# Kernel tuning notes

Hardware: AMD Instinct MI355X
Metric: run time of the kernel (lower is better)

The kernel has to match this reference:

```python
import jax, jax.numpy as jnp
import numpy as np

B, N, M = 8, 2048, 2048
DQ = DK = DV = H = O = 1024

def setup_inputs() -> dict:
    key = jax.random.key(0)
    ks = jax.random.split(key, 10)
    input_query = jax.random.normal(ks[0], (B, N, DQ), dtype=jnp.float32)
    input_key = jax.random.normal(ks[1], (B, M, DK), dtype=jnp.float32)
    input_value = jax.random.normal(ks[2], (B, M, DV), dtype=jnp.float32)
    seq_lens = jax.random.randint(ks[3], (B,), 1, M + 1)
    seq_lens = seq_lens.at[0].set(M)  # original asserts max(seq_lens) == M
    s = 1.0 / np.sqrt(DQ)
    Wq = jax.random.normal(ks[4], (DQ, H), dtype=jnp.float32) * s
    bq = jnp.zeros((H,), dtype=jnp.float32)
    Wk = jax.random.normal(ks[5], (DK, H), dtype=jnp.float32) * s
    bk = jnp.zeros((H,), dtype=jnp.float32)
    Wv = jax.random.normal(ks[6], (DV, O), dtype=jnp.float32) * s
    bv = jnp.zeros((O,), dtype=jnp.float32)
    return {"input_query": input_query, "input_key": input_key, "input_value": input_value,
            "seq_lens": seq_lens, "Wq": Wq, "bq": bq, "Wk": Wk, "bk": bk, "Wv": Wv, "bv": bv}


def reference(input_query, input_key, input_value, seq_lens, Wq, bq, Wk, bk, Wv, bv):
    hidden_dim = Wq.shape[1]
    lq = input_query @ Wq + bq          # (B, N, H)
    lk = input_key @ Wk + bk            # (B, M, H)
    lv = input_value @ Wv + bv          # (B, M, O)
    scores = jnp.einsum('bnh,bmh->bnm', lq, lk) / jnp.sqrt(jnp.float32(hidden_dim))
    # additive mask: 0 for valid positions, finfo.min for padded (as in original)
    valid = (jnp.arange(scores.shape[-1]) < seq_lens[:, None])[:, None, :]  # (B,1,M)
    add_mask = jnp.where(valid, 0.0, jnp.finfo(scores.dtype).min)
    scores = scores + add_mask
    probs = jax.nn.softmax(scores, axis=-1)
    out = jnp.einsum('bnm,bmo->bno', probs, lv)  # dropout is identity in eval
    return out
```

## Files before the change

kernel.cpp:

```cpp
#include <hip/hip_runtime.h>
#include <hip/hip_bf16.h>

typedef unsigned short u16;
typedef __attribute__((ext_vector_type(8))) short bfrag;
typedef __attribute__((ext_vector_type(4))) float f32x4;
typedef __attribute__((ext_vector_type(8))) unsigned short us8;
typedef __attribute__((ext_vector_type(4))) unsigned short us4;

__device__ __forceinline__ u16 f2bf(float f) {
  union { float f; unsigned int u; } x; x.f = f;
  unsigned int r = x.u + 0x7fffu + ((x.u >> 16) & 1u);
  return (u16)(r >> 16);
}
__device__ __forceinline__ float bf2f(u16 u) {
  union { unsigned int u; float f; } x; x.u = ((unsigned int)u) << 16;
  return x.f;
}

__device__ __forceinline__ void gld16(const void* g, void* l) {
  __builtin_amdgcn_global_load_lds((const __attribute__((address_space(1))) void*)g,
                                   (__attribute__((address_space(3))) void*)l, 16, 0, 0);
}

__global__ __launch_bounds__(256) void transpose_w(const float* __restrict__ W0,
                                                   const float* __restrict__ W1,
                                                   const float* __restrict__ W2,
                                                   u16* __restrict__ T0,
                                                   u16* __restrict__ T1,
                                                   u16* __restrict__ T2) {
  const float* W = (blockIdx.z == 0) ? W0 : ((blockIdx.z == 1) ? W1 : W2);
  u16* T = (blockIdx.z == 0) ? T0 : ((blockIdx.z == 1) ? T1 : T2);
  __shared__ u16 tile[64][72];
  const int t = threadIdx.x;
  const int rr = t >> 4;
  const int cc = (t & 15) * 4;
  const int kbase = blockIdx.y * 64, nbase = blockIdx.x * 64;
#pragma unroll
  for (int j = 0; j < 4; ++j) {
    int kl = rr + j * 16;
    float4 v = *(const float4*)(W + (size_t)(kbase + kl) * 1024 + nbase + cc);
    tile[kl][cc + 0] = f2bf(v.x);
    tile[kl][cc + 1] = f2bf(v.y);
    tile[kl][cc + 2] = f2bf(v.z);
    tile[kl][cc + 3] = f2bf(v.w);
  }
  __syncthreads();
#pragma unroll
  for (int j = 0; j < 4; ++j) {
    int nl = rr + j * 16;
    us4 o;
    o[0] = tile[cc + 0][nl];
    o[1] = tile[cc + 1][nl];
    o[2] = tile[cc + 2][nl];
    o[3] = tile[cc + 3][nl];
    *(us4*)(T + (size_t)(nbase + nl) * 1024 + kbase + cc) = o;
  }
}

__global__ __launch_bounds__(256) void cvt_bf16(const float* __restrict__ src,
                                                u16* __restrict__ dst, int n8) {
  int i = blockIdx.x * blockDim.x + threadIdx.x;
  const int stride = gridDim.x * blockDim.x;
  for (; i < n8; i += stride) {
    const float4* p = (const float4*)(src + (size_t)i * 8);
    float4 v0 = p[0], v1 = p[1];
    us8 o;
    o[0] = f2bf(v0.x); o[1] = f2bf(v0.y); o[2] = f2bf(v0.z); o[3] = f2bf(v0.w);
    o[4] = f2bf(v1.x); o[5] = f2bf(v1.y); o[6] = f2bf(v1.z); o[7] = f2bf(v1.w);
    *(us8*)(dst + (size_t)i * 8) = o;
  }
}

template <int OUT>
__global__ __launch_bounds__(512, 2) void gemm256(const u16* __restrict__ gA,
                                                  const u16* __restrict__ gB,
                                                  const float* __restrict__ bias,
                                                  void* __restrict__ outp,
                                                  int K, int ldc,
                                                  size_t aStride, size_t bStride,
                                                  size_t cStride,
                                                  const int* __restrict__ seq) {
  __shared__ u16 lds[65536];
  const int tid = threadIdx.x;

  const int id = blockIdx.x + gridDim.x * (blockIdx.y + gridDim.y * blockIdx.z);
  int bx, by, bz;
  if constexpr (OUT == 0 || OUT == 2) {
    bx = (id >> 3) & 3; by = (id & 7) + 8 * (id >> 5); bz = 0;
  } else if constexpr (OUT == 1) {
    bx = (id >> 3) & 7; by = id & 7; bz = id >> 6;
  } else {
    bx = (id >> 3) & 3; by = id & 7; bz = id >> 5;
  }

  const u16* A = gA + (size_t)bz * aStride;
  const u16* B = gB + (size_t)bz * bStride;
  const int brow = by * 256, bcol = bx * 256;

  const int NT = K >> 6;
  int NTe = NT;
  if constexpr (OUT == 1) {
    if (bcol >= seq[bz]) return;
  }
  if constexpr (OUT == 3) {
    const int len = seq[bz];
    const int nt2 = (len + 63) >> 6;
    NTe = nt2 < NT ? nt2 : NT;
  }

  const int wv = tid >> 6, l = tid & 63;
  const int wm = wv >> 2, wn = wv & 3;
  const int fr = l & 15, fq = l >> 4;
  const int g0 = (fq ^ (fr & 7)) * 8;
  const int g1 = ((4 + fq) ^ (fr & 7)) * 8;

  const int srow = tid >> 3;
  const int sg = (tid & 7) ^ (srow & 7);
  const u16* aS = A + (size_t)(brow + srow) * K + sg * 8;
  const u16* bS = B + (size_t)(bcol + srow) * K + sg * 8;
  u16* const dA = lds + wv * 512;
  u16* const dB = lds + 32768 + wv * 512;

  f32x4 acc[8][4] = {};

  auto stA = [&](int tile, int c, int buf) {
    gld16(aS + (size_t)tile * 64 + (size_t)c * 64 * K, dA + buf * 16384 + c * 4096);
  };
  auto stB = [&](int tile, int c, int buf) {
    gld16(bS + (size_t)tile * 64 + (size_t)c * 64 * K, dB + buf * 16384 + c * 4096);
  };

#pragma unroll
  for (int c = 0; c < 4; ++c) stA(0, c, 0);
#pragma unroll
  for (int c = 0; c < 4; ++c) stB(0, c, 0);
  if (NTe > 1) {
    stA(1, 0, 1); stA(1, 2, 1);
    stB(1, 0, 1); stB(1, 1, 1); stB(1, 2, 1); stB(1, 3, 1);
  }

  for (int t = 0; t < NTe; ++t) {
    const int cur = t & 1;
    const u16* At = lds + cur * 16384;
    const u16* Bt = lds + 32768 + cur * 16384;

    if (t + 1 < NTe) asm volatile("s_waitcnt vmcnt(6)" ::: "memory");
    else             asm volatile("s_waitcnt vmcnt(0)" ::: "memory");
    __builtin_amdgcn_s_barrier();

    bfrag a[4][2], b[2][2][2];

#pragma unroll
    for (int m = 0; m < 4; ++m) {
      const u16* p = At + (wm * 128 + m * 16 + fr) * 64;
      a[m][0] = *(const bfrag*)(p + g0);
      a[m][1] = *(const bfrag*)(p + g1);
    }
#pragma unroll
    for (int n = 0; n < 2; ++n) {
      const u16* p = Bt + (wn * 64 + n * 16 + fr) * 64;
      b[0][n][0] = *(const bfrag*)(p + g0);
      b[0][n][1] = *(const bfrag*)(p + g1);
    }
    if (t + 1 < NTe) { stA(t + 1, 1, cur ^ 1); stA(t + 1, 3, cur ^ 1); }
    __builtin_amdgcn_s_barrier();
    asm volatile("s_waitcnt lgkmcnt(0)" ::: "memory");
    __builtin_amdgcn_sched_barrier(0);
    __builtin_amdgcn_s_setprio(1);
#pragma unroll
    for (int n = 0; n < 2; ++n)
#pragma unroll
      for (int m = 0; m < 4; ++m) {
        acc[m][n] = __builtin_amdgcn_mfma_f32_16x16x32_bf16(a[m][0], b[0][n][0], acc[m][n], 0, 0, 0);
        acc[m][n] = __builtin_amdgcn_mfma_f32_16x16x32_bf16(a[m][1], b[0][n][1], acc[m][n], 0, 0, 0);
      }
    __builtin_amdgcn_s_setprio(0);
    __builtin_amdgcn_s_barrier();

#pragma unroll
    for (int n = 0; n < 2; ++n) {
      const u16* p = Bt + (wn * 64 + 32 + n * 16 + fr) * 64;
      b[1][n][0] = *(const bfrag*)(p + g0);
      b[1][n][1] = *(const bfrag*)(p + g1);
    }
    if (t + 2 < NTe) { stA(t + 2, 0, cur); stA(t + 2, 2, cur); }
    __builtin_amdgcn_s_barrier();
    asm volatile("s_waitcnt lgkmcnt(0)" ::: "memory");
    __builtin_amdgcn_sched_barrier(0);
    __builtin_amdgcn_s_setprio(1);
#pragma unroll
    for (int n = 0; n < 2; ++n)
#pragma unroll
      for (int m = 0; m < 4; ++m) {
        acc[m][2 + n] = __builtin_amdgcn_mfma_f32_16x16x32_bf16(a[m][0], b[1][n][0], acc[m][2 + n], 0, 0, 0);
        acc[m][2 + n] = __builtin_amdgcn_mfma_f32_16x16x32_bf16(a[m][1], b[1][n][1], acc[m][2 + n], 0, 0, 0);
      }
    __builtin_amdgcn_s_setprio(0);
    __builtin_amdgcn_s_barrier();

#pragma unroll
    for (int m = 0; m < 4; ++m) {
      const u16* p = At + (wm * 128 + 64 + m * 16 + fr) * 64;
      a[m][0] = *(const bfrag*)(p + g0);
      a[m][1] = *(const bfrag*)(p + g1);
    }
    if (t + 2 < NTe) { stB(t + 2, 0, cur); stB(t + 2, 1, cur); }
    __builtin_amdgcn_s_barrier();
    asm volatile("s_waitcnt lgkmcnt(0)" ::: "memory");
    __builtin_amdgcn_sched_barrier(0);
    __builtin_amdgcn_s_setprio(1);
#pragma unroll
    for (int n = 0; n < 2; ++n)
#pragma unroll
      for (int m = 0; m < 4; ++m) {
        acc[4 + m][n] = __builtin_amdgcn_mfma_f32_16x16x32_bf16(a[m][0], b[0][n][0], acc[4 + m][n], 0, 0, 0);
        acc[4 + m][n] = __builtin_amdgcn_mfma_f32_16x16x32_bf16(a[m][1], b[0][n][1], acc[4 + m][n], 0, 0, 0);
      }
    __builtin_amdgcn_s_setprio(0);
    __builtin_amdgcn_s_barrier();

    if (t + 2 < NTe) { stB(t + 2, 2, cur); stB(t + 2, 3, cur); }
    __builtin_amdgcn_s_setprio(1);
#pragma unroll
    for (int n = 0; n < 2; ++n)
#pragma unroll
      for (int m = 0; m < 4; ++m) {
        acc[4 + m][2 + n] = __builtin_amdgcn_mfma_f32_16x16x32_bf16(a[m][0], b[1][n][0], acc[4 + m][2 + n], 0, 0, 0);
        acc[4 + m][2 + n] = __builtin_amdgcn_mfma_f32_16x16x32_bf16(a[m][1], b[1][n][1], acc[4 + m][2 + n], 0, 0, 0);
      }
    __builtin_amdgcn_s_setprio(0);
  }

#pragma unroll
  for (int mg = 0; mg < 8; ++mg) {
    const int r0 = brow + wm * 128 + mg * 16 + fq * 4;
#pragma unroll
    for (int n = 0; n < 4; ++n) {
      const int c = bcol + wn * 64 + n * 16 + fr;
      f32x4 vv = acc[mg][n];
      if constexpr (OUT == 0) {
        float bb = bias[c];
        u16* C = (u16*)outp;
#pragma unroll
        for (int j = 0; j < 4; ++j) C[(size_t)(r0 + j) * ldc + c] = f2bf(vv[j] + bb);
      } else if constexpr (OUT == 1) {
        u16* C = (u16*)outp + (size_t)bz * cStride;
#pragma unroll
        for (int j = 0; j < 4; ++j) C[(size_t)(r0 + j) * ldc + c] = f2bf(vv[j] * 0.03125f);
      } else if constexpr (OUT == 2) {
        float bb = bias[c];
        const int bz2 = r0 >> 11, mm = r0 & 2047;
        us4 o;
#pragma unroll
        for (int j = 0; j < 4; ++j) o[j] = f2bf(vv[j] + bb);
        *(us4*)((u16*)outp + ((size_t)bz2 * 1024 + c) * 2048 + mm) = o;
      } else {
        float* C = (float*)outp + (size_t)bz * cStride;
#pragma unroll
        for (int j = 0; j < 4; ++j) C[(size_t)(r0 + j) * ldc + c] = vv[j];
      }
    }
  }
}

__global__ __launch_bounds__(256) void softmax_mask(u16* __restrict__ probs,
                                                    const int* __restrict__ seq) {
  const int bid = blockIdx.x;
  const int b = bid >> 11, n = bid & 2047;
  const int len = seq[b];
  const int len64 = (len + 63) & ~63;
  u16* row = probs + ((size_t)b * 2048 + n) * 2048;
  const int t = threadIdx.x;
  const int w = t >> 6, l = t & 63;

  us8 sv = {};
  if (t * 8 < len) sv = *(const us8*)(row + t * 8);
  float vals[8];
  float vmax = -1e30f;
#pragma unroll
  for (int e = 0; e < 8; ++e) {
    int m = t * 8 + e;
    float x = bf2f(sv[e]);
    vals[e] = (m < len) ? x : -1e30f;
    vmax = fmaxf(vmax, vals[e]);
  }
#pragma unroll
  for (int o = 32; o > 0; o >>= 1) vmax = fmaxf(vmax, __shfl_xor(vmax, o, 64));
  __shared__ float sm[4], ss[4];
  if (l == 0) sm[w] = vmax;
  __syncthreads();
  vmax = fmaxf(fmaxf(sm[0], sm[1]), fmaxf(sm[2], sm[3]));

  float ev[8];
  float sum = 0.f;
#pragma unroll
  for (int e = 0; e < 8; ++e) {
    int m = t * 8 + e;
    float p = (m < len) ? __expf(vals[e] - vmax) : 0.f;
    ev[e] = p;
    sum += p;
  }
#pragma unroll
  for (int o = 32; o > 0; o >>= 1) sum += __shfl_xor(sum, o, 64);
  if (l == 0) ss[w] = sum;
  __syncthreads();
  sum = ss[0] + ss[1] + ss[2] + ss[3];
  float inv = 1.f / sum;
  if (t * 8 < len64) {
    us8 ov;
#pragma unroll
    for (int e = 0; e < 8; ++e) ov[e] = f2bf(ev[e] * inv);
    *(us8*)(row + t * 8) = ov;
  }
}

extern "C" void kernel_launch(void* const* d_in, const int* in_sizes, int n_in,
                              void* d_out, int out_size, void* d_ws, size_t ws_size,
                              hipStream_t stream) {
  const float* q   = (const float*)d_in[0];
  const float* k   = (const float*)d_in[1];
  const float* v   = (const float*)d_in[2];
  const int*   seq = (const int*)d_in[3];
  const float* Wq  = (const float*)d_in[4];
  const float* bq  = (const float*)d_in[5];
  const float* Wk  = (const float*)d_in[6];
  const float* bk  = (const float*)d_in[7];
  const float* Wv  = (const float*)d_in[8];
  const float* bv  = (const float*)d_in[9];
  float* out = (float*)d_out;

  u16* ws = (u16*)d_ws;
  u16* wtq = ws;
  u16* wtk = wtq + (size_t)1024 * 1024;
  u16* wtv = wtk + (size_t)1024 * 1024;
  u16* lq  = wtv + (size_t)1024 * 1024;
  u16* lk  = lq + (size_t)16384 * 1024;
  u16* lvt = lk + (size_t)16384 * 1024;
  u16* probs = lvt + (size_t)16384 * 1024;
  u16* cbuf = probs;

  const size_t S21 = (size_t)2048 * 1024;
  const size_t S22 = (size_t)2048 * 2048;

  transpose_w<<<dim3(16, 16, 3), 256, 0, stream>>>(Wq, Wk, Wv, wtq, wtk, wtv);

  cvt_bf16<<<dim3(2048), 256, 0, stream>>>(q, cbuf, 2097152);
  gemm256<0><<<dim3(4, 64, 1), 512, 0, stream>>>(cbuf, wtq, bq, lq, 1024, 1024, 0, 0, 0, nullptr);
  cvt_bf16<<<dim3(2048), 256, 0, stream>>>(k, cbuf, 2097152);
  gemm256<0><<<dim3(4, 64, 1), 512, 0, stream>>>(cbuf, wtk, bk, lk, 1024, 1024, 0, 0, 0, nullptr);
  cvt_bf16<<<dim3(2048), 256, 0, stream>>>(v, cbuf, 2097152);
  gemm256<2><<<dim3(4, 64, 1), 512, 0, stream>>>(cbuf, wtv, bv, lvt, 1024, 1024, 0, 0, 0, nullptr);

  gemm256<1><<<dim3(8, 8, 8), 512, 0, stream>>>(lq, lk, nullptr, probs, 1024, 2048, S21, S21, S22, seq);
  softmax_mask<<<dim3(16384), 256, 0, stream>>>(probs, seq);
  gemm256<3><<<dim3(4, 8, 8), 512, 0, stream>>>(probs, lvt, nullptr, out, 2048, 1024, S22, S21, S21, seq);
}
```

Measured before the change: 320.8 us.

## Use smaller 128x128 tiled GEMM kernel for attention score and output matmuls

Adds a new gemm128d kernel with 128x128 tiles, simple double buffering and 4 blocks per CU, and uses it for the QK^T scores and the probs@V output, which take the seq_len-dependent early exit and K truncation. The smaller tiles give finer skipping of masked columns and more blocks for the batched GEMMs. This should improve load balance across batches with short sequences. The 256 kernel is simplified to projection-only use and gains a trailing barrier per iteration. The cost is lower per-block data reuse and a simpler pipeline that waits on global loads every tile.

```diff
diff --git a/kernel.cpp b/kernel.cpp
--- a/kernel.cpp
+++ b/kernel.cpp
@@ -76,37 +76,16 @@
                                                   const u16* __restrict__ gB,
                                                   const float* __restrict__ bias,
                                                   void* __restrict__ outp,
-                                                  int K, int ldc,
-                                                  size_t aStride, size_t bStride,
-                                                  size_t cStride,
-                                                  const int* __restrict__ seq) {
+                                                  int K, int ldc) {
   __shared__ u16 lds[65536];
   const int tid = threadIdx.x;
 
-  const int id = blockIdx.x + gridDim.x * (blockIdx.y + gridDim.y * blockIdx.z);
-  int bx, by, bz;
-  if constexpr (OUT == 0 || OUT == 2) {
-    bx = (id >> 3) & 3; by = (id & 7) + 8 * (id >> 5); bz = 0;
-  } else if constexpr (OUT == 1) {
-    bx = (id >> 3) & 7; by = id & 7; bz = id >> 6;
-  } else {
-    bx = (id >> 3) & 3; by = id & 7; bz = id >> 5;
-  }
-
-  const u16* A = gA + (size_t)bz * aStride;
-  const u16* B = gB + (size_t)bz * bStride;
+  const int id = blockIdx.x + gridDim.x * blockIdx.y;
+  const int bx = (id >> 3) & 3, by = (id & 7) + 8 * (id >> 5);
+
+  const u16* A = gA;
+  const u16* B = gB;
   const int brow = by * 256, bcol = bx * 256;
-
-  const int NT = K >> 6;
-  int NTe = NT;
-  if constexpr (OUT == 1) {
-    if (bcol >= seq[bz]) return;
-  }
-  if constexpr (OUT == 3) {
-    const int len = seq[bz];
-    const int nt2 = (len + 63) >> 6;
-    NTe = nt2 < NT ? nt2 : NT;
-  }
 
   const int wv = tid >> 6, l = tid & 63;
   const int wm = wv >> 2, wn = wv & 3;
@@ -122,6 +101,7 @@
   u16* const dB = lds + 32768 + wv * 512;
 
   f32x4 acc[8][4] = {};
+  const int NT = K >> 6;
 
   auto stA = [&](int tile, int c, int buf) {
     gld16(aS + (size_t)tile * 64 + (size_t)c * 64 * K, dA + buf * 16384 + c * 4096);
@@ -134,18 +114,18 @@
   for (int c = 0; c < 4; ++c) stA(0, c, 0);
 #pragma unroll
   for (int c = 0; c < 4; ++c) stB(0, c, 0);
-  if (NTe > 1) {
+  if (NT > 1) {
     stA(1, 0, 1); stA(1, 2, 1);
     stB(1, 0, 1); stB(1, 1, 1); stB(1, 2, 1); stB(1, 3, 1);
   }
 
-  for (int t = 0; t < NTe; ++t) {
+  for (int t = 0; t < NT; ++t) {
     const int cur = t & 1;
     const u16* At = lds + cur * 16384;
     const u16* Bt = lds + 32768 + cur * 16384;
 
-    if (t + 1 < NTe) asm volatile("s_waitcnt vmcnt(6)" ::: "memory");
-    else             asm volatile("s_waitcnt vmcnt(0)" ::: "memory");
+    if (t + 1 < NT) asm volatile("s_waitcnt vmcnt(6)" ::: "memory");
+    else            asm volatile("s_waitcnt vmcnt(0)" ::: "memory");
     __builtin_amdgcn_s_barrier();
 
     bfrag a[4][2], b[2][2][2];
@@ -162,7 +142,7 @@
       b[0][n][0] = *(const bfrag*)(p + g0);
       b[0][n][1] = *(const bfrag*)(p + g1);
     }
-    if (t + 1 < NTe) { stA(t + 1, 1, cur ^ 1); stA(t + 1, 3, cur ^ 1); }
+    if (t + 1 < NT) { stA(t + 1, 1, cur ^ 1); stA(t + 1, 3, cur ^ 1); }
     __builtin_amdgcn_s_barrier();
     asm volatile("s_waitcnt lgkmcnt(0)" ::: "memory");
     __builtin_amdgcn_sched_barrier(0);
@@ -183,7 +163,7 @@
       b[1][n][0] = *(const bfrag*)(p + g0);
       b[1][n][1] = *(const bfrag*)(p + g1);
     }
-    if (t + 2 < NTe) { stA(t + 2, 0, cur); stA(t + 2, 2, cur); }
+    if (t + 2 < NT) { stA(t + 2, 0, cur); stA(t + 2, 2, cur); }
     __builtin_amdgcn_s_barrier();
     asm volatile("s_waitcnt lgkmcnt(0)" ::: "memory");
     __builtin_amdgcn_sched_barrier(0);
@@ -204,7 +184,7 @@
       a[m][0] = *(const bfrag*)(p + g0);
       a[m][1] = *(const bfrag*)(p + g1);
     }
-    if (t + 2 < NTe) { stB(t + 2, 0, cur); stB(t + 2, 1, cur); }
+    if (t + 2 < NT) { stB(t + 2, 0, cur); stB(t + 2, 1, cur); }
     __builtin_amdgcn_s_barrier();
     asm volatile("s_waitcnt lgkmcnt(0)" ::: "memory");
     __builtin_amdgcn_sched_barrier(0);
@@ -219,7 +199,7 @@
     __builtin_amdgcn_s_setprio(0);
     __builtin_amdgcn_s_barrier();
 
-    if (t + 2 < NTe) { stB(t + 2, 2, cur); stB(t + 2, 3, cur); }
+    if (t + 2 < NT) { stB(t + 2, 2, cur); stB(t + 2, 3, cur); }
     __builtin_amdgcn_s_setprio(1);
 #pragma unroll
     for (int n = 0; n < 2; ++n)
@@ -229,6 +209,7 @@
         acc[4 + m][2 + n] = __builtin_amdgcn_mfma_f32_16x16x32_bf16(a[m][1], b[1][n][1], acc[4 + m][2 + n], 0, 0, 0);
       }
     __builtin_amdgcn_s_setprio(0);
+    __builtin_amdgcn_s_barrier();
   }
 
 #pragma unroll
@@ -238,22 +219,121 @@
     for (int n = 0; n < 4; ++n) {
       const int c = bcol + wn * 64 + n * 16 + fr;
       f32x4 vv = acc[mg][n];
+      float bb = bias[c];
       if constexpr (OUT == 0) {
-        float bb = bias[c];
         u16* C = (u16*)outp;
 #pragma unroll
         for (int j = 0; j < 4; ++j) C[(size_t)(r0 + j) * ldc + c] = f2bf(vv[j] + bb);
-      } else if constexpr (OUT == 1) {
-        u16* C = (u16*)outp + (size_t)bz * cStride;
-#pragma unroll
-        for (int j = 0; j < 4; ++j) C[(size_t)(r0 + j) * ldc + c] = f2bf(vv[j] * 0.03125f);
-      } else if constexpr (OUT == 2) {
-        float bb = bias[c];
+      } else {
         const int bz2 = r0 >> 11, mm = r0 & 2047;
         us4 o;
 #pragma unroll
         for (int j = 0; j < 4; ++j) o[j] = f2bf(vv[j] + bb);
         *(us4*)((u16*)outp + ((size_t)bz2 * 1024 + c) * 2048 + mm) = o;
+      }
+    }
+  }
+}
+
+template <int OUT>
+__global__ __launch_bounds__(512, 4) void gemm128d(const u16* __restrict__ gA,
+                                                   const u16* __restrict__ gB,
+                                                   void* __restrict__ outp,
+                                                   int K, int ldc,
+                                                   size_t aStride, size_t bStride,
+                                                   size_t cStride,
+                                                   const int* __restrict__ seq) {
+  __shared__ u16 lds[32768];
+  const int tid = threadIdx.x;
+  const int bx = blockIdx.x, by = blockIdx.y, bz = blockIdx.z;
+
+  const u16* A = gA + (size_t)bz * aStride;
+  const u16* B = gB + (size_t)bz * bStride;
+  const int brow = by * 128, bcol = bx * 128;
+
+  int NTe = K >> 6;
+  if constexpr (OUT == 1) {
+    if (bcol >= seq[bz]) return;
+  }
+  if constexpr (OUT == 3) {
+    const int nt2 = (seq[bz] + 63) >> 6;
+    NTe = nt2 < NTe ? nt2 : NTe;
+  }
+
+  const int wv = tid >> 6, l = tid & 63;
+  const int wm = wv >> 2, wn = wv & 3;
+  const int fr = l & 15, fq = l >> 4;
+  const int g0 = (fq ^ (fr & 7)) * 8;
+  const int g1 = ((4 + fq) ^ (fr & 7)) * 8;
+
+  const int srow = tid >> 3;
+  const int sg = (tid & 7) ^ (srow & 7);
+  const u16* aS = A + (size_t)(brow + srow) * K + sg * 8;
+  const u16* bS = B + (size_t)(bcol + srow) * K + sg * 8;
+  u16* const dA = lds + wv * 512;
+  u16* const dB = lds + 16384 + wv * 512;
+
+  f32x4 acc[4][2] = {};
+
+  auto stage = [&](int tile, int buf) {
+#pragma unroll
+    for (int c = 0; c < 2; ++c)
+      gld16(aS + (size_t)tile * 64 + (size_t)c * 64 * K, dA + buf * 8192 + c * 4096);
+#pragma unroll
+    for (int c = 0; c < 2; ++c)
+      gld16(bS + (size_t)tile * 64 + (size_t)c * 64 * K, dB + buf * 8192 + c * 4096);
+  };
+
+  stage(0, 0);
+  asm volatile("s_waitcnt vmcnt(0)" ::: "memory");
+  __builtin_amdgcn_s_barrier();
+
+  for (int t = 0; t < NTe; ++t) {
+    const int cur = t & 1;
+    const u16* At = lds + cur * 8192;
+    const u16* Bt = lds + 16384 + cur * 8192;
+
+    if (t + 1 < NTe) stage(t + 1, cur ^ 1);
+
+    bfrag a[4][2], b[2][2];
+#pragma unroll
+    for (int m = 0; m < 4; ++m) {
+      const u16* p = At + (wm * 64 + m * 16 + fr) * 64;
+      a[m][0] = *(const bfrag*)(p + g0);
+      a[m][1] = *(const bfrag*)(p + g1);
+    }
+#pragma unroll
+    for (int n = 0; n < 2; ++n) {
+      const u16* p = Bt + (wn * 32 + n * 16 + fr) * 64;
+      b[n][0] = *(const bfrag*)(p + g0);
+      b[n][1] = *(const bfrag*)(p + g1);
+    }
+    asm volatile("s_waitcnt lgkmcnt(0)" ::: "memory");
+    __builtin_amdgcn_sched_barrier(0);
+    __builtin_amdgcn_s_setprio(1);
+#pragma unroll
+    for (int m = 0; m < 4; ++m)
+#pragma unroll
+      for (int n = 0; n < 2; ++n) {
+        acc[m][n] = __builtin_amdgcn_mfma_f32_16x16x32_bf16(a[m][0], b[n][0], acc[m][n], 0, 0, 0);
+        acc[m][n] = __builtin_amdgcn_mfma_f32_16x16x32_bf16(a[m][1], b[n][1], acc[m][n], 0, 0, 0);
+      }
+    __builtin_amdgcn_s_setprio(0);
+    if (t + 1 < NTe) asm volatile("s_waitcnt vmcnt(0)" ::: "memory");
+    __builtin_amdgcn_s_barrier();
+  }
+
+#pragma unroll
+  for (int m = 0; m < 4; ++m) {
+    const int r0 = brow + wm * 64 + m * 16 + fq * 4;
+#pragma unroll
+    for (int n = 0; n < 2; ++n) {
+      const int c = bcol + wn * 32 + n * 16 + fr;
+      f32x4 vv = acc[m][n];
+      if constexpr (OUT == 1) {
+        u16* C = (u16*)outp + (size_t)bz * cStride;
+#pragma unroll
+        for (int j = 0; j < 4; ++j) C[(size_t)(r0 + j) * ldc + c] = f2bf(vv[j] * 0.03125f);
       } else {
         float* C = (float*)outp + (size_t)bz * cStride;
 #pragma unroll
@@ -345,13 +425,13 @@
   transpose_w<<<dim3(16, 16, 3), 256, 0, stream>>>(Wq, Wk, Wv, wtq, wtk, wtv);
 
   cvt_bf16<<<dim3(2048), 256, 0, stream>>>(q, cbuf, 2097152);
-  gemm256<0><<<dim3(4, 64, 1), 512, 0, stream>>>(cbuf, wtq, bq, lq, 1024, 1024, 0, 0, 0, nullptr);
+  gemm256<0><<<dim3(4, 64, 1), 512, 0, stream>>>(cbuf, wtq, bq, lq, 1024, 1024);
   cvt_bf16<<<dim3(2048), 256, 0, stream>>>(k, cbuf, 2097152);
-  gemm256<0><<<dim3(4, 64, 1), 512, 0, stream>>>(cbuf, wtk, bk, lk, 1024, 1024, 0, 0, 0, nullptr);
+  gemm256<0><<<dim3(4, 64, 1), 512, 0, stream>>>(cbuf, wtk, bk, lk, 1024, 1024);
   cvt_bf16<<<dim3(2048), 256, 0, stream>>>(v, cbuf, 2097152);
-  gemm256<2><<<dim3(4, 64, 1), 512, 0, stream>>>(cbuf, wtv, bv, lvt, 1024, 1024, 0, 0, 0, nullptr);
-
-  gemm256<1><<<dim3(8, 8, 8), 512, 0, stream>>>(lq, lk, nullptr, probs, 1024, 2048, S21, S21, S22, seq);
+  gemm256<2><<<dim3(4, 64, 1), 512, 0, stream>>>(cbuf, wtv, bv, lvt, 1024, 1024);
+
+  gemm128d<1><<<dim3(16, 16, 8), 512, 0, stream>>>(lq, lk, probs, 1024, 2048, S21, S21, S22, seq);
   softmax_mask<<<dim3(16384), 256, 0, stream>>>(probs, seq);
-  gemm256<3><<<dim3(4, 8, 8), 512, 0, stream>>>(probs, lvt, nullptr, out, 2048, 1024, S22, S21, S21, seq);
-}
+  gemm128d<3><<<dim3(8, 16, 8), 512, 0, stream>>>(probs, lvt, out, 2048, 1024, S22, S21, S21, seq);
+}
```

Measured after the change: 328.4 us. +2.4%, slower.
